# Performance work log

Hardware: AMD Instinct MI355X
Metric: run time of the kernel (lower is better)

Reference implementation:

```python
import jax, jax.numpy as jnp
import numpy as np

Q = 2.0
TEMPERATURE = 1.0
EXP = 1.0 / (Q - 1.0)  # exponent 1/(q-1); q=2 -> sparsemax-style projection
N_BISECT_ITERS = 50    # enough for xtol ~ 1e-6 over an interval of width ~ (u_max - u_min + 10)


def setup_inputs() -> dict:
    key = jax.random.key(0)
    k_x, k_w1, k_w2 = jax.random.split(key, 3)
    B, D, H, E = 8192, 4096, 256, 64
    x = jax.random.normal(k_x, (B, D), dtype=jnp.float32)
    w1 = jax.random.normal(k_w1, (D, H), dtype=jnp.float32) * 0.02
    b1 = jnp.zeros((H,), dtype=jnp.float32)
    w2 = jax.random.normal(k_w2, (H, E), dtype=jnp.float32) * 0.05
    b2 = jnp.zeros((E,), dtype=jnp.float32)
    return {"x": x, "w1": w1, "b1": b1, "w2": w2, "b2": b2}


def _bisect_tau(us):
    # us: [B, E] = utilities / temperature. Find per-row tau with sum(relu(us - tau)**EXP) = 1.
    lo = jnp.min(us, axis=-1) - 10.0   # constraint(lo) > 0
    hi = jnp.max(us, axis=-1)          # constraint(hi) = -1 < 0

    def body(i, carry):
        lo, hi = carry
        mid = 0.5 * (lo + hi)
        f = jnp.sum(jnp.maximum(us - mid[..., None], 0.0) ** EXP, axis=-1) - 1.0
        pos = f > 0.0  # constraint is decreasing in tau: root is above mid
        return (jnp.where(pos, mid, lo), jnp.where(pos, hi, mid))

    lo, hi = jax.lax.fori_loop(0, N_BISECT_ITERS, body, (lo, hi))
    return 0.5 * (lo + hi)  # [B]


def reference(x, w1, b1, w2, b2):
    # utility_net (Dropout is identity in eval mode)
    h = jax.nn.relu(x @ w1 + b1)            # [B, 256]
    utilities = h @ w2 + b2                  # [B, E]
    us = utilities / TEMPERATURE
    # tau is found by root-finding on detached values in the original (.item()),
    # so it is a constant w.r.t. differentiation.
    tau = jax.lax.stop_gradient(_bisect_tau(jax.lax.stop_gradient(us)))
    p = jnp.maximum(us - tau[..., None], 0.0) ** EXP   # [B, E]
    p = p / (jnp.sum(p, axis=-1, keepdims=True) + 1e-8)
    return p
```

## Files before the change

### kernel.cpp

```cpp
#include <hip/hip_runtime.h>
#include <stdint.h>

typedef _Float16 f16;
typedef _Float16 f16x8 __attribute__((ext_vector_type(8)));
typedef _Float16 f16x4 __attribute__((ext_vector_type(4)));
typedef float f32x4 __attribute__((ext_vector_type(4)));

#define D_DIM 4096
#define H_DIM 256
#define E_DIM 64
#define BM 128
#define BK 64
#define KSPLIT 4
#define NKT2 16
#define HP_SLICE (8192 * 256)

__global__ void pack_kernel(const float* __restrict__ w1, f16* __restrict__ w1s,
                            const float* __restrict__ w2, f16* __restrict__ w2s) {
  const int b = blockIdx.x;
  const int t = threadIdx.x;
  if (b < 512) {
    const int u = b * 256 + t;
    const int lane = u & 63;
    const int kk = (u >> 6) & 1;
    const int c16 = (u >> 7) & 15;
    const int kt = u >> 11;
    const int g = lane >> 4, r = lane & 15;
    const int k0 = kt * 64 + kk * 32 + g * 8;
    const int col = c16 * 16 + r;
    f16x8 o;
#pragma unroll
    for (int j = 0; j < 8; ++j) o[j] = (f16)w1[(size_t)(k0 + j) * H_DIM + col];
    *(f16x8*)(w1s + (size_t)u * 8) = o;
  } else {
    const int u = (b - 512) * 256 + t;
    const int lane = u & 63;
    const int ks = (u >> 6) & 7;
    const int cg = u >> 9;
    const int g = lane >> 4, r = lane & 15;
    const int k0 = ks * 32 + g * 8;
    const int col = cg * 16 + r;
    f16x8 o;
#pragma unroll
    for (int j = 0; j < 8; ++j) o[j] = (f16)w2[(size_t)(k0 + j) * E_DIM + col];
    *(f16x8*)(w2s + (size_t)u * 8) = o;
  }
}

__launch_bounds__(512, 2)
__global__ void gemm1_splitk_kernel(const float* __restrict__ x,
                                    const f16* __restrict__ w1s,
                                    float* __restrict__ hpart) {
  __shared__ __align__(16) f16 buf0[BM * BK];
  __shared__ __align__(16) f16 buf1[BM * BK];

  const int t = threadIdx.x;
  const int lane = t & 63;
  const int wn = t >> 6;
  const int wm = wn >> 2;
  const int wc = wn & 3;
  const int g = lane >> 4, r = lane & 15;
  const int bid = blockIdx.x;
  const int ks = bid & 3;
  const int brow = (bid >> 2) * BM;
  const int kph = (bid * 5) & 15;

#define KT(s) ((kph + (s)) & 15)

  const float* xb = x + (size_t)(brow + (t >> 4)) * D_DIM + ks * 1024 + ((t & 15) << 2);
  const int stw_swz = (((t & 15) << 2) ^ (((t >> 4) & 7) << 3));
  const int stw_row0 = (t >> 4);

  const f16* bptr = w1s + (size_t)ks * (16 * 16384) + (size_t)(wc * 8) * 512 + lane * 8;

  f32x4 acc[4][4];
#pragma unroll
  for (int mf = 0; mf < 4; ++mf)
#pragma unroll
    for (int nf = 0; nf < 4; ++nf) acc[mf][nf] = (f32x4){0.f, 0.f, 0.f, 0.f};

  f16x8 BE[8], BO[8];
  float4 xA[4], xB[4], xP[4];

#define LDX(kt, xr)                                                     \
  {                                                                     \
    _Pragma("unroll") for (int i = 0; i < 4; ++i)                       \
      (xr)[i] = *(const float4*)(xb + (size_t)i * (32 * D_DIM) + (kt) * 64); \
  }
#define LDB(kt, B)                                                      \
  {                                                                     \
    const f16* p_ = bptr + (size_t)(kt) * 16384;                        \
    _Pragma("unroll") for (int q = 0; q < 8; ++q)                       \
      (B)[q] = *(const f16x8*)(p_ + q * 512);                           \
  }
#define STW(dst, xr)                                                    \
  {                                                                     \
    _Pragma("unroll") for (int i = 0; i < 4; ++i) {                     \
      f16x4 hv_;                                                        \
      hv_[0] = (f16)(xr)[i].x; hv_[1] = (f16)(xr)[i].y;                 \
      hv_[2] = (f16)(xr)[i].z; hv_[3] = (f16)(xr)[i].w;                 \
      *(f16x4*)((dst) + (i * 32 + stw_row0) * 64 + stw_swz) = hv_;      \
    }                                                                   \
  }
#define COMP(buf, B)                                                           \
  {                                                                            \
    _Pragma("unroll") for (int kk = 0; kk < 2; ++kk) {                         \
      const int kb_ = (kk * 32 + g * 8) ^ ((r & 7) << 3);                      \
      _Pragma("unroll") for (int mf = 0; mf < 4; ++mf) {                       \
        const int row_ = wm * 64 + mf * 16 + r;                                \
        const f16x8 af_ = *(const f16x8*)((buf) + row_ * 64 + kb_);            \
        _Pragma("unroll") for (int nf = 0; nf < 4; ++nf) {                     \
          acc[mf][nf] = __builtin_amdgcn_mfma_f32_16x16x32_f16(                \
              af_, (B)[nf * 2 + kk], acc[mf][nf], 0, 0, 0);                    \
        }                                                                      \
      }                                                                        \
    }                                                                          \
  }
#define BAR()                                          \
  asm volatile("s_waitcnt lgkmcnt(0)" ::: "memory");   \
  __builtin_amdgcn_s_barrier();

  {
    LDX(KT(0), xP);
    LDB(KT(0), BE);
    LDB(KT(1), BO);
    LDX(KT(1), xA);
    LDX(KT(2), xB);
    STW(buf0, xP);
    BAR();
  }

#pragma unroll 1
  for (int it = 0; it < NKT2 / 2; ++it) {
    const int s = it * 2;
    STW(buf1, xA);
    LDX(KT(s + 3), xA);
    COMP(buf0, BE);
    LDB(KT(s + 2), BE);
    BAR();
    STW(buf0, xB);
    LDX(KT(s + 4), xB);
    COMP(buf1, BO);
    LDB(KT(s + 3), BO);
    BAR();
  }

  float* hp = hpart + (size_t)ks * HP_SLICE + (size_t)brow * H_DIM;
#pragma unroll
  for (int mf = 0; mf < 4; ++mf)
#pragma unroll
    for (int nf = 0; nf < 4; ++nf) {
      const int col = wc * 64 + nf * 16 + r;
#pragma unroll
      for (int j = 0; j < 4; ++j) {
        const int row = wm * 64 + mf * 16 + g * 4 + j;
        hp[(size_t)row * H_DIM + col] = acc[mf][nf][j];
      }
    }
}

__launch_bounds__(512)
__global__ void reduce_fused_kernel(const float* __restrict__ hpart,
                                    const float* __restrict__ b1,
                                    const f16* __restrict__ w2s,
                                    const float* __restrict__ b2,
                                    float* __restrict__ out) {
  __shared__ __align__(16) char smem[24576];
  f16* h_lds = (f16*)smem;
  float* u_lds = (float*)(smem + 16384);

  const int t = threadIdx.x;
  const int lane = t & 63;
  const int wn = t >> 6;
  const int g = lane >> 4, r = lane & 15;
  const int brow = blockIdx.x * 32;

  const float* base = hpart + (size_t)brow * H_DIM;
  float4 s[4];
#pragma unroll
  for (int i = 0; i < 4; ++i)
    s[i] = *(const float4*)(base + (size_t)(i * 512 + t) * 4);
#pragma unroll
  for (int c = 1; c < KSPLIT; ++c) {
    const float* cb = base + (size_t)c * HP_SLICE;
#pragma unroll
    for (int i = 0; i < 4; ++i) {
      const float4 v = *(const float4*)(cb + (size_t)(i * 512 + t) * 4);
      s[i].x += v.x; s[i].y += v.y; s[i].z += v.z; s[i].w += v.w;
    }
  }
#pragma unroll
  for (int i = 0; i < 4; ++i) {
    const int f = i * 512 + t;
    const int row = f >> 6;
    const int col = (f & 63) << 2;
    const float4 bv = *(const float4*)(b1 + col);
    f16x4 hv;
    hv[0] = (f16)fmaxf(s[i].x + bv.x, 0.f);
    hv[1] = (f16)fmaxf(s[i].y + bv.y, 0.f);
    hv[2] = (f16)fmaxf(s[i].z + bv.z, 0.f);
    hv[3] = (f16)fmaxf(s[i].w + bv.w, 0.f);
    *(f16x4*)(h_lds + row * 256 + (col ^ ((row & 7) << 3))) = hv;
  }
  __syncthreads();

  const int rh2 = wn & 1;
  const int cg = wn >> 1;
  f32x4 acc2 = {0.f, 0.f, 0.f, 0.f};
  const f16* w2p = w2s + (size_t)(cg * 8) * 512 + lane * 8;
#pragma unroll
  for (int ksi = 0; ksi < 8; ++ksi) {
    const int arow = rh2 * 16 + r;
    const int kb = ksi * 32 + g * 8;
    const f16x8 af = *(const f16x8*)(h_lds + arow * 256 + (kb ^ ((arow & 7) << 3)));
    const f16x8 bf = *(const f16x8*)(w2p + ksi * 512);
    acc2 = __builtin_amdgcn_mfma_f32_16x16x32_f16(af, bf, acc2, 0, 0, 0);
  }
  {
    const int col = cg * 16 + r;
    const float bias = b2[col];
#pragma unroll
    for (int j = 0; j < 4; ++j) {
      const int row = rh2 * 16 + g * 4 + j;
      u_lds[row * 64 + col] = acc2[j] + bias;
    }
  }
  __syncthreads();

  const int srow = wn * 4 + (lane >> 4);
  const int scol = (lane & 15) << 2;
  const float4 uv = *(const float4*)(u_lds + srow * 64 + scol);
  float u0 = uv.x, u1 = uv.y, u2 = uv.z, u3 = uv.w;

  float mx = fmaxf(fmaxf(u0, u1), fmaxf(u2, u3));
  float mn = fminf(fminf(u0, u1), fminf(u2, u3));
#pragma unroll
  for (int m = 1; m < 16; m <<= 1) {
    mx = fmaxf(mx, __shfl_xor(mx, m));
    mn = fminf(mn, __shfl_xor(mn, m));
  }
  float lo = mn - 10.0f, hi = mx;
#pragma unroll 1
  for (int it = 0; it < 32; ++it) {
    const float mid = 0.5f * (lo + hi);
    float sm = fmaxf(u0 - mid, 0.f) + fmaxf(u1 - mid, 0.f) +
               fmaxf(u2 - mid, 0.f) + fmaxf(u3 - mid, 0.f);
#pragma unroll
    for (int m = 1; m < 16; m <<= 1) sm += __shfl_xor(sm, m);
    const bool pos = (sm - 1.0f) > 0.0f;
    lo = pos ? mid : lo;
    hi = pos ? hi : mid;
  }
  const float tau = 0.5f * (lo + hi);
  const float p0 = fmaxf(u0 - tau, 0.f);
  const float p1 = fmaxf(u1 - tau, 0.f);
  const float p2 = fmaxf(u2 - tau, 0.f);
  const float p3 = fmaxf(u3 - tau, 0.f);
  float sum = p0 + p1 + p2 + p3;
#pragma unroll
  for (int m = 1; m < 16; m <<= 1) sum += __shfl_xor(sum, m);
  const float inv = 1.0f / (sum + 1e-8f);
  float4 pv;
  pv.x = p0 * inv; pv.y = p1 * inv; pv.z = p2 * inv; pv.w = p3 * inv;
  *(float4*)(out + (size_t)(brow + srow) * E_DIM + scol) = pv;
}

extern "C" void kernel_launch(void* const* d_in, const int* in_sizes, int n_in,
                              void* d_out, int out_size, void* d_ws, size_t ws_size,
                              hipStream_t stream) {
  const float* x  = (const float*)d_in[0];
  const float* w1 = (const float*)d_in[1];
  const float* b1 = (const float*)d_in[2];
  const float* w2 = (const float*)d_in[3];
  const float* b2 = (const float*)d_in[4];
  float* out = (float*)d_out;

  char* wsb = (char*)d_ws;
  f16* w1s = (f16*)wsb;
  f16* w2s = (f16*)(wsb + (2u << 20));
  float* hpart = (float*)(wsb + (4u << 20));

  pack_kernel<<<520, 256, 0, stream>>>(w1, w1s, w2, w2s);
  gemm1_splitk_kernel<<<256, 512, 0, stream>>>(x, w1s, hpart);
  reduce_fused_kernel<<<256, 512, 0, stream>>>(hpart, b1, w2s, b2, out);
}
```

Measured before the change: 58.22 us.

## Stream x tiles via global_load_lds into a 4-stage fp32 LDS ring; fp16 split-K partials

The GEMM1 kernel now loads fp32 x tiles straight into a 4-deep LDS ring using global_load_lds with an XOR swizzle. The fp16 conversion moves to the point where MFMA operands are read, and vmcnt-based waits replace the register staging and LDS store pass. This removes register pressure and the VGPR-to-LDS copy, and gives deeper prefetch. Split-K partial sums are also stored as fp16 instead of fp32, which halves the partial write and read traffic in the reduce kernel. The cost is 128KB of LDS per block, which likely caps occupancy at one block per CU, plus reduced precision in the partial sums.

```diff
diff --git a/kernel.cpp b/kernel.cpp
--- a/kernel.cpp
+++ b/kernel.cpp
@@ -3,14 +3,12 @@
 
 typedef _Float16 f16;
 typedef _Float16 f16x8 __attribute__((ext_vector_type(8)));
-typedef _Float16 f16x4 __attribute__((ext_vector_type(4)));
 typedef float f32x4 __attribute__((ext_vector_type(4)));
 
 #define D_DIM 4096
 #define H_DIM 256
 #define E_DIM 64
 #define BM 128
-#define BK 64
 #define KSPLIT 4
 #define NKT2 16
 #define HP_SLICE (8192 * 256)
@@ -50,26 +48,25 @@
 __launch_bounds__(512, 2)
 __global__ void gemm1_splitk_kernel(const float* __restrict__ x,
                                     const f16* __restrict__ w1s,
-                                    float* __restrict__ hpart) {
-  __shared__ __align__(16) f16 buf0[BM * BK];
-  __shared__ __align__(16) f16 buf1[BM * BK];
+                                    f16* __restrict__ hpart) {
+  __shared__ __align__(16) float xbuf[4][BM * 64];
 
   const int t = threadIdx.x;
   const int lane = t & 63;
   const int wn = t >> 6;
-  const int wm = wn >> 2;
-  const int wc = wn & 3;
+  const int wm = wn >> 2, wc = wn & 3;
   const int g = lane >> 4, r = lane & 15;
   const int bid = blockIdx.x;
   const int ks = bid & 3;
   const int brow = (bid >> 2) * BM;
   const int kph = (bid * 5) & 15;
-
 #define KT(s) ((kph + (s)) & 15)
 
-  const float* xb = x + (size_t)(brow + (t >> 4)) * D_DIM + ks * 1024 + ((t & 15) << 2);
-  const int stw_swz = (((t & 15) << 2) ^ (((t >> 4) & 7) << 3));
-  const int stw_row0 = (t >> 4);
+  const int drow = lane >> 4;
+  int hbo[4];
+#pragma unroll
+  for (int i = 0; i < 4; ++i) hbo[i] = ((lane & 15) ^ ((i * 4 + drow) & 15)) * 4;
+  const float* dbase = x + (size_t)(brow + wn * 16 + drow) * D_DIM + ks * 1024;
 
   const f16* bptr = w1s + (size_t)ks * (16 * 16384) + (size_t)(wc * 8) * 512 + lane * 8;
 
@@ -80,12 +77,16 @@
     for (int nf = 0; nf < 4; ++nf) acc[mf][nf] = (f32x4){0.f, 0.f, 0.f, 0.f};
 
   f16x8 BE[8], BO[8];
-  float4 xA[4], xB[4], xP[4];
-
-#define LDX(kt, xr)                                                     \
-  {                                                                     \
-    _Pragma("unroll") for (int i = 0; i < 4; ++i)                       \
-      (xr)[i] = *(const float4*)(xb + (size_t)i * (32 * D_DIM) + (kt) * 64); \
+
+#define GLDS(bufidx, kt)                                                        \
+  {                                                                             \
+    _Pragma("unroll") for (int i = 0; i < 4; ++i) {                             \
+      const float* gp_ = dbase + (size_t)(i * 4) * D_DIM + (kt) * 64 + hbo[i];  \
+      __builtin_amdgcn_global_load_lds(                                         \
+          (const __attribute__((address_space(1))) void*)gp_,                   \
+          (__attribute__((address_space(3))) void*)&xbuf[bufidx][(wn * 4 + i) * 256], \
+          16, 0, 0);                                                            \
+    }                                                                           \
   }
 #define LDB(kt, B)                                                      \
   {                                                                     \
@@ -93,59 +94,60 @@
     _Pragma("unroll") for (int q = 0; q < 8; ++q)                       \
       (B)[q] = *(const f16x8*)(p_ + q * 512);                           \
   }
-#define STW(dst, xr)                                                    \
-  {                                                                     \
-    _Pragma("unroll") for (int i = 0; i < 4; ++i) {                     \
-      f16x4 hv_;                                                        \
-      hv_[0] = (f16)(xr)[i].x; hv_[1] = (f16)(xr)[i].y;                 \
-      hv_[2] = (f16)(xr)[i].z; hv_[3] = (f16)(xr)[i].w;                 \
-      *(f16x4*)((dst) + (i * 32 + stw_row0) * 64 + stw_swz) = hv_;      \
-    }                                                                   \
-  }
-#define COMP(buf, B)                                                           \
-  {                                                                            \
-    _Pragma("unroll") for (int kk = 0; kk < 2; ++kk) {                         \
-      const int kb_ = (kk * 32 + g * 8) ^ ((r & 7) << 3);                      \
-      _Pragma("unroll") for (int mf = 0; mf < 4; ++mf) {                       \
-        const int row_ = wm * 64 + mf * 16 + r;                                \
-        const f16x8 af_ = *(const f16x8*)((buf) + row_ * 64 + kb_);            \
-        _Pragma("unroll") for (int nf = 0; nf < 4; ++nf) {                     \
-          acc[mf][nf] = __builtin_amdgcn_mfma_f32_16x16x32_f16(                \
-              af_, (B)[nf * 2 + kk], acc[mf][nf], 0, 0, 0);                    \
-        }                                                                      \
-      }                                                                        \
-    }                                                                          \
-  }
-#define BAR()                                          \
-  asm volatile("s_waitcnt lgkmcnt(0)" ::: "memory");   \
-  __builtin_amdgcn_s_barrier();
-
-  {
-    LDX(KT(0), xP);
-    LDB(KT(0), BE);
-    LDB(KT(1), BO);
-    LDX(KT(1), xA);
-    LDX(KT(2), xB);
-    STW(buf0, xP);
-    BAR();
-  }
+#define COMP(bufidx, B)                                                         \
+  {                                                                             \
+    _Pragma("unroll") for (int kk = 0; kk < 2; ++kk) {                          \
+      _Pragma("unroll") for (int mf = 0; mf < 4; ++mf) {                        \
+        const int row_ = wm * 64 + mf * 16 + r;                                 \
+        const float* bp_ = &xbuf[bufidx][row_ * 64];                            \
+        const int L0_ = kk * 8 + g * 2;                                         \
+        const float4 a0_ = *(const float4*)(bp_ + ((L0_ ^ r) << 2));            \
+        const float4 a1_ = *(const float4*)(bp_ + (((L0_ + 1) ^ r) << 2));      \
+        f16x8 af_;                                                              \
+        af_[0] = (f16)a0_.x; af_[1] = (f16)a0_.y;                               \
+        af_[2] = (f16)a0_.z; af_[3] = (f16)a0_.w;                               \
+        af_[4] = (f16)a1_.x; af_[5] = (f16)a1_.y;                               \
+        af_[6] = (f16)a1_.z; af_[7] = (f16)a1_.w;                               \
+        _Pragma("unroll") for (int nf = 0; nf < 4; ++nf)                        \
+          acc[mf][nf] = __builtin_amdgcn_mfma_f32_16x16x32_f16(                 \
+              af_, (B)[nf * 2 + kk], acc[mf][nf], 0, 0, 0);                     \
+      }                                                                         \
+    }                                                                           \
+  }
+#define STEP(s, bidx, B)                                  \
+  {                                                       \
+    GLDS(((s) + 2) & 3, KT((s) + 2));                     \
+    asm volatile("s_waitcnt vmcnt(16)" ::: "memory");     \
+    __builtin_amdgcn_s_barrier();                         \
+    COMP(bidx, B);                                        \
+    LDB(KT((s) + 2), B);                                  \
+  }
+#define STEPN(s, bidx, B, WAIT)                           \
+  {                                                       \
+    asm volatile(WAIT ::: "memory");                      \
+    __builtin_amdgcn_s_barrier();                         \
+    COMP(bidx, B);                                        \
+  }
+
+  GLDS(0, KT(0));
+  LDB(KT(0), BE);
+  GLDS(1, KT(1));
+  LDB(KT(1), BO);
 
 #pragma unroll 1
-  for (int it = 0; it < NKT2 / 2; ++it) {
-    const int s = it * 2;
-    STW(buf1, xA);
-    LDX(KT(s + 3), xA);
-    COMP(buf0, BE);
-    LDB(KT(s + 2), BE);
-    BAR();
-    STW(buf0, xB);
-    LDX(KT(s + 4), xB);
-    COMP(buf1, BO);
-    LDB(KT(s + 3), BO);
-    BAR();
-  }
-
-  float* hp = hpart + (size_t)ks * HP_SLICE + (size_t)brow * H_DIM;
+  for (int q = 0; q < 3; ++q) {
+    const int s0 = q * 4;
+    STEP(s0 + 0, 0, BE);
+    STEP(s0 + 1, 1, BO);
+    STEP(s0 + 2, 2, BE);
+    STEP(s0 + 3, 3, BO);
+  }
+  STEP(12, 0, BE);
+  STEP(13, 1, BO);
+  STEPN(14, 2, BE, "s_waitcnt vmcnt(12)");
+  STEPN(15, 3, BO, "s_waitcnt vmcnt(0)");
+
+  f16* hp = hpart + (size_t)ks * HP_SLICE + (size_t)brow * H_DIM;
 #pragma unroll
   for (int mf = 0; mf < 4; ++mf)
 #pragma unroll
@@ -154,13 +156,13 @@
 #pragma unroll
       for (int j = 0; j < 4; ++j) {
         const int row = wm * 64 + mf * 16 + g * 4 + j;
-        hp[(size_t)row * H_DIM + col] = acc[mf][nf][j];
+        hp[(size_t)row * H_DIM + col] = (f16)acc[mf][nf][j];
       }
     }
 }
 
 __launch_bounds__(512)
-__global__ void reduce_fused_kernel(const float* __restrict__ hpart,
+__global__ void reduce_fused_kernel(const f16* __restrict__ hpart,
                                     const float* __restrict__ b1,
                                     const f16* __restrict__ w2s,
                                     const float* __restrict__ b2,
@@ -175,32 +177,29 @@
   const int g = lane >> 4, r = lane & 15;
   const int brow = blockIdx.x * 32;
 
-  const float* base = hpart + (size_t)brow * H_DIM;
-  float4 s[4];
-#pragma unroll
-  for (int i = 0; i < 4; ++i)
-    s[i] = *(const float4*)(base + (size_t)(i * 512 + t) * 4);
-#pragma unroll
-  for (int c = 1; c < KSPLIT; ++c) {
-    const float* cb = base + (size_t)c * HP_SLICE;
-#pragma unroll
-    for (int i = 0; i < 4; ++i) {
-      const float4 v = *(const float4*)(cb + (size_t)(i * 512 + t) * 4);
-      s[i].x += v.x; s[i].y += v.y; s[i].z += v.z; s[i].w += v.w;
+  const int row = t >> 4;
+  const int col0 = (t & 15) << 4;
+  const f16* base = hpart + (size_t)(brow + row) * H_DIM + col0;
+  float a[16];
+#pragma unroll
+  for (int j = 0; j < 16; ++j) a[j] = 0.f;
+#pragma unroll
+  for (int c = 0; c < KSPLIT; ++c) {
+    const f16x8 va = *(const f16x8*)(base + (size_t)c * HP_SLICE);
+    const f16x8 vb = *(const f16x8*)(base + (size_t)c * HP_SLICE + 8);
+#pragma unroll
+    for (int j = 0; j < 8; ++j) { a[j] += (float)va[j]; a[8 + j] += (float)vb[j]; }
+  }
+  {
+    const int s8 = (row & 7) << 3;
+    f16x8 h0, h1;
+#pragma unroll
+    for (int j = 0; j < 8; ++j) {
+      h0[j] = (f16)fmaxf(a[j] + b1[col0 + j], 0.f);
+      h1[j] = (f16)fmaxf(a[8 + j] + b1[col0 + 8 + j], 0.f);
     }
-  }
-#pragma unroll
-  for (int i = 0; i < 4; ++i) {
-    const int f = i * 512 + t;
-    const int row = f >> 6;
-    const int col = (f & 63) << 2;
-    const float4 bv = *(const float4*)(b1 + col);
-    f16x4 hv;
-    hv[0] = (f16)fmaxf(s[i].x + bv.x, 0.f);
-    hv[1] = (f16)fmaxf(s[i].y + bv.y, 0.f);
-    hv[2] = (f16)fmaxf(s[i].z + bv.z, 0.f);
-    hv[3] = (f16)fmaxf(s[i].w + bv.w, 0.f);
-    *(f16x4*)(h_lds + row * 256 + (col ^ ((row & 7) << 3))) = hv;
+    *(f16x8*)(h_lds + row * 256 + (col0 ^ s8)) = h0;
+    *(f16x8*)(h_lds + row * 256 + ((col0 + 8) ^ s8)) = h1;
   }
   __syncthreads();
 
@@ -221,8 +220,8 @@
     const float bias = b2[col];
 #pragma unroll
     for (int j = 0; j < 4; ++j) {
-      const int row = rh2 * 16 + g * 4 + j;
-      u_lds[row * 64 + col] = acc2[j] + bias;
+      const int rr = rh2 * 16 + g * 4 + j;
+      u_lds[rr * 64 + col] = acc2[j] + bias;
     }
   }
   __syncthreads();
@@ -278,7 +277,7 @@
   char* wsb = (char*)d_ws;
   f16* w1s = (f16*)wsb;
   f16* w2s = (f16*)(wsb + (2u << 20));
-  float* hpart = (float*)(wsb + (4u << 20));
+  f16* hpart = (f16*)(wsb + (4u << 20));
 
   pack_kernel<<<520, 256, 0, stream>>>(w1, w1s, w2, w2s);
   gemm1_splitk_kernel<<<256, 512, 0, stream>>>(x, w1s, hpart);
```

Result: faster. 53.07 us (-8.9%).
